# Kernel optimization log

Hardware: AMD Instinct MI355X
Metric: run time of the kernel (lower is better)

The kernel has to match this reference:

```python
import jax, jax.numpy as jnp
import numpy as np

N = 8192
D = 64
NUM_CLASSES = 100


def setup_inputs() -> dict:
    key = jax.random.key(0)
    k1, k2 = jax.random.split(key)
    output = jax.random.normal(k1, (N, D), dtype=jnp.float32)
    target = jax.random.randint(k2, (N,), 0, NUM_CLASSES, dtype=jnp.int64)
    return {"output": output, "target": target}


def reference(output, target):
    n = output.shape[0]
    # Pairwise similarity logits: [n, n]
    sim = output @ output.T
    # Upper-triangular (i < j) pair indices, static for jit.
    iu, ju = np.triu_indices(n, k=1)
    iu = jnp.asarray(iu)
    ju = jnp.asarray(ju)
    logits = sim[iu, ju]                                  # [n*(n-1)/2]
    labels = (target[iu] == target[ju]).astype(logits.dtype)
    # BCEWithLogits, mean reduction (numerically stable via log_sigmoid).
    loss = -(labels * jax.nn.log_sigmoid(logits)
             + (1.0 - labels) * jax.nn.log_sigmoid(-logits))
    return jnp.mean(loss)
```

## Files before the change

kernel.cpp:

```cpp
#include <hip/hip_runtime.h>

typedef __attribute__((ext_vector_type(8))) short bf16x8;
typedef __attribute__((ext_vector_type(4))) float floatx4;

namespace {
constexpr int kN = 8192;
constexpr int kD = 64;
constexpr int kTile = 128;
constexpr int kTilesPerDim = kN / kTile;
constexpr int kNumBlocks = kTilesPerDim * (kTilesPerDim + 1) / 2;
constexpr double kNumPairs = (double)kN * (double)(kN - 1) / 2.0;
__device__ __constant__ float kA1 = 0.99949556f;
__device__ __constant__ float kA2 = -0.49190896f;
__device__ __constant__ float kA3 = 0.28947478f;
__device__ __constant__ float kA4 = -0.13606275f;
__device__ __constant__ float kA5 = 0.03215845f;
constexpr float kNegLog2e = -1.4426950408889634f;
}

__device__ __forceinline__ short f2bf(float f) {
  unsigned u = __builtin_bit_cast(unsigned, f);
  unsigned r = u + 0x7FFFu + ((u >> 16) & 1u);
  return (short)(r >> 16);
}

__device__ __forceinline__ bf16x8 cvt8(const float4 f0, const float4 f1) {
  bf16x8 v;
  v[0] = f2bf(f0.x); v[1] = f2bf(f0.y); v[2] = f2bf(f0.z); v[3] = f2bf(f0.w);
  v[4] = f2bf(f1.x); v[5] = f2bf(f1.y); v[6] = f2bf(f1.z); v[7] = f2bf(f1.w);
  return v;
}

__device__ __forceinline__ float fast_exp2(float t) {
#if __has_builtin(__builtin_amdgcn_exp2f)
  return __builtin_amdgcn_exp2f(t);
#else
  return exp2f(t);
#endif
}

__global__ __launch_bounds__(256, 4) void pair_loss_kernel(
    const float* __restrict__ feat, const int* __restrict__ tgt,
    float* __restrict__ partial) {
  __shared__ short Bs[kTile * kD];
  __shared__ int Tcol[kTile];
  __shared__ float Red[4];

  const int bid = blockIdx.x;
  int by;
  {
    float f = 0.5f * (129.0f - sqrtf(16641.0f - 8.0f * (float)bid));
    by = (int)f;
    by = by > 63 ? 63 : (by < 0 ? 0 : by);
    while (64 * (by + 1) - ((by + 1) * by) / 2 <= bid) ++by;
    while (64 * by - (by * (by - 1)) / 2 > bid) --by;
  }
  const int bx = by + (bid - (64 * by - (by * (by - 1)) / 2));

  const int tid = threadIdx.x;
  const int lane = tid & 63;
  const int w = tid >> 6;
  const int quad = lane >> 4;
  const int l15 = lane & 15;
  const int l7 = lane & 7;

  {
    const int c = tid & 7;
    const int r0 = tid >> 3;
#pragma unroll
    for (int i = 0; i < 4; ++i) {
      const int r = r0 + 32 * i;
      const float* src = feat + (size_t)(bx * kTile + r) * kD + c * 8;
      const float4 f0 = *(const float4*)src;
      const float4 f1 = *(const float4*)(src + 4);
      *(bf16x8*)&Bs[r * kD + ((c ^ (r & 7)) << 3)] = cvt8(f0, f1);
    }
    if (tid < kTile) Tcol[tid] = tgt[bx * kTile + tid];
  }

  const int arow = by * kTile + w * 32;
  bf16x8 afrag[2][2];
#pragma unroll
  for (int rb = 0; rb < 2; ++rb) {
    const int row = arow + rb * 16 + l15;
#pragma unroll
    for (int ks = 0; ks < 2; ++ks) {
      const float* src = feat + (size_t)row * kD + ks * 32 + quad * 8;
      afrag[rb][ks] = cvt8(*(const float4*)src, *(const float4*)(src + 4));
    }
  }

  int trow[2][4];
#pragma unroll
  for (int rb = 0; rb < 2; ++rb) {
    const int4 t4 = *(const int4*)(tgt + arow + rb * 16 + quad * 4);
    trow[rb][0] = t4.x; trow[rb][1] = t4.y; trow[rb][2] = t4.z; trow[rb][3] = t4.w;
  }

  __syncthreads();

  float S_x = 0.0f, S_a = 0.0f, S_l = 0.0f, S_y = 0.0f;

#pragma unroll 2
  for (int cb = 0; cb < 8; ++cb) {
    const int R = cb * 16 + l15;
    const bf16x8 b0 = *(const bf16x8*)&Bs[R * kD + ((quad ^ l7) << 3)];
    const bf16x8 b1 = *(const bf16x8*)&Bs[R * kD + (((4 + quad) ^ l7) << 3)];
    floatx4 acc0 = {0.f, 0.f, 0.f, 0.f};
    floatx4 acc1 = {0.f, 0.f, 0.f, 0.f};
    acc0 = __builtin_amdgcn_mfma_f32_16x16x32_bf16(afrag[0][0], b0, acc0, 0, 0, 0);
    acc0 = __builtin_amdgcn_mfma_f32_16x16x32_bf16(afrag[0][1], b1, acc0, 0, 0, 0);
    acc1 = __builtin_amdgcn_mfma_f32_16x16x32_bf16(afrag[1][0], b0, acc1, 0, 0, 0);
    acc1 = __builtin_amdgcn_mfma_f32_16x16x32_bf16(afrag[1][1], b1, acc1, 0, 0, 0);

    const int tc = Tcol[R];
#pragma unroll
    for (int rb = 0; rb < 2; ++rb) {
      const floatx4 a = rb ? acc1 : acc0;
#pragma unroll
      for (int reg = 0; reg < 4; ++reg) {
        const float x = a[reg];
        S_x += x;
        S_a += fabsf(x);
        const float e = fast_exp2(kNegLog2e * fabsf(x));
        float h = fmaf(e, kA5, kA4);
        h = fmaf(e, h, kA3);
        h = fmaf(e, h, kA2);
        h = fmaf(e, h, kA1);
        S_l = fmaf(e, h, S_l);
        if (trow[rb][reg] == tc) S_y += x;
      }
    }
  }

  float lsum = 0.5f * (S_x + S_a) + S_l - S_y;

#pragma unroll
  for (int off = 32; off > 0; off >>= 1) lsum += __shfl_down(lsum, off);
  if (lane == 0) Red[w] = lsum;
  __syncthreads();
  if (tid == 0) {
    const float scale =
        (float)(1.0 / kNumPairs) * ((bx == by) ? 0.5f : 1.0f);
    partial[bid] = (Red[0] + Red[1] + Red[2] + Red[3]) * scale;
  }
}

__global__ void reduce_kernel(const float* __restrict__ partial,
                              float* __restrict__ out) {
  __shared__ float ws[4];
  const int tid = threadIdx.x;
  float s = 0.0f;
  for (int i = tid; i < kNumBlocks; i += 256) s += partial[i];
#pragma unroll
  for (int off = 32; off > 0; off >>= 1) s += __shfl_down(s, off);
  if ((tid & 63) == 0) ws[tid >> 6] = s;
  __syncthreads();
  if (tid == 0) out[0] = ws[0] + ws[1] + ws[2] + ws[3];
}

extern "C" void kernel_launch(void* const* d_in, const int* in_sizes, int n_in,
                              void* d_out, int out_size, void* d_ws,
                              size_t ws_size, hipStream_t stream) {
  const float* feat = (const float*)d_in[0];
  const int* tgt = (const int*)d_in[1];
  float* partial = (float*)d_ws;

  pair_loss_kernel<<<kNumBlocks, 256, 0, stream>>>(feat, tgt, partial);
  reduce_kernel<<<1, 256, 0, stream>>>(partial, (float*)d_out);
}
```

Measured before the change: 78.56 us.

## Replace per-pair label and linear terms with closed-form class-sum algebra

The linear parts of the loss (sum of x and the same-label sum of x) are computed algebraically from the feature sum vector and per-class feature sums, built by new class-sum and reduce kernels. This removes the per-pair target comparison and the per-element linear accumulation. The pair kernel now processes 128x256 tiles using a new block mapping that zero-weights tiles below the diagonal, and the final kernel combines the pieces. This adds two extra launches and shared-memory atomics, and introduces cancellation risk in float32 from subtracting large quadratic terms.

```diff
diff --git a/kernel.cpp b/kernel.cpp
--- a/kernel.cpp
+++ b/kernel.cpp
@@ -7,8 +7,9 @@
 constexpr int kN = 8192;
 constexpr int kD = 64;
 constexpr int kTile = 128;
-constexpr int kTilesPerDim = kN / kTile;
-constexpr int kNumBlocks = kTilesPerDim * (kTilesPerDim + 1) / 2;
+constexpr int kNumClasses = 100;
+constexpr int kNumBlocks = 1056;
+constexpr int kClsBlocks = 64;
 constexpr double kNumPairs = (double)kN * (double)(kN - 1) / 2.0;
 __device__ __constant__ float kA1 = 0.99949556f;
 __device__ __constant__ float kA2 = -0.49190896f;
@@ -16,6 +17,11 @@
 __device__ __constant__ float kA4 = -0.13606275f;
 __device__ __constant__ float kA5 = 0.03215845f;
 constexpr float kNegLog2e = -1.4426950408889634f;
+constexpr float kNegHalfLn2 = -0.34657359027997264f;
+constexpr int kOffG = 0;
+constexpr int kOffCls = 4096;
+constexpr int kOffSvec = kOffCls + kClsBlocks * kNumClasses * kD;
+constexpr int kOffClsSq = kOffSvec + kD;
 }
 
 __device__ __forceinline__ short f2bf(float f) {
@@ -39,23 +45,64 @@
 #endif
 }
 
+__global__ __launch_bounds__(256) void class_sum_kernel(
+    const float* __restrict__ feat, const int* __restrict__ tgt, float* ws) {
+  __shared__ float cls[kNumClasses * kD];
+  const int tid = threadIdx.x;
+  const int b = blockIdx.x;
+  for (int i = tid; i < kNumClasses * kD; i += 256) cls[i] = 0.0f;
+  if (b == 0 && tid < kD + 1) {
+    if (tid < kD) ws[kOffSvec + tid] = 0.0f;
+    else ws[kOffClsSq] = 0.0f;
+  }
+  __syncthreads();
+
+  const int row = b * 128 + (tid >> 1);
+  const int half = (tid & 1) * 32;
+  const int t = tgt[row];
+  const float* src = feat + (size_t)row * kD + half;
+#pragma unroll
+  for (int v = 0; v < 8; ++v) {
+    const float4 f = *(const float4*)(src + v * 4);
+    atomicAdd(&cls[t * kD + half + v * 4 + 0], f.x);
+    atomicAdd(&cls[t * kD + half + v * 4 + 1], f.y);
+    atomicAdd(&cls[t * kD + half + v * 4 + 2], f.z);
+    atomicAdd(&cls[t * kD + half + v * 4 + 3], f.w);
+  }
+  __syncthreads();
+  float* out = ws + kOffCls + (size_t)b * kNumClasses * kD;
+  for (int i = tid; i < kNumClasses * kD; i += 256) out[i] = cls[i];
+}
+
+__global__ __launch_bounds__(256) void class_reduce_kernel(float* ws) {
+  __shared__ float red[4];
+  const int tid = threadIdx.x;
+  const int gid = blockIdx.x * 256 + tid;
+  float s = 0.0f;
+  for (int b = 0; b < kClsBlocks; ++b)
+    s += ws[kOffCls + (size_t)b * kNumClasses * kD + gid];
+  atomicAdd(&ws[kOffSvec + (gid & (kD - 1))], s);
+  float q = s * s;
+#pragma unroll
+  for (int off = 32; off > 0; off >>= 1) q += __shfl_down(q, off);
+  if ((tid & 63) == 0) red[tid >> 6] = q;
+  __syncthreads();
+  if (tid == 0) atomicAdd(&ws[kOffClsSq], red[0] + red[1] + red[2] + red[3]);
+}
+
 __global__ __launch_bounds__(256, 4) void pair_loss_kernel(
-    const float* __restrict__ feat, const int* __restrict__ tgt,
-    float* __restrict__ partial) {
-  __shared__ short Bs[kTile * kD];
-  __shared__ int Tcol[kTile];
+    const float* __restrict__ feat, float* __restrict__ ws) {
+  __shared__ short Bs[256 * kD];
   __shared__ float Red[4];
 
   const int bid = blockIdx.x;
-  int by;
-  {
-    float f = 0.5f * (129.0f - sqrtf(16641.0f - 8.0f * (float)bid));
-    by = (int)f;
-    by = by > 63 ? 63 : (by < 0 ? 0 : by);
-    while (64 * (by + 1) - ((by + 1) * by) / 2 <= bid) ++by;
-    while (64 * by - (by * (by - 1)) / 2 > bid) --by;
-  }
-  const int bx = by + (bid - (64 * by - (by * (by - 1)) / 2));
+  int by = 0, start = 0;
+  while (start + (32 - (by >> 1)) <= bid) {
+    start += 32 - (by >> 1);
+    ++by;
+  }
+  const int sc = (by >> 1) + (bid - start);
+  const int bx0 = 2 * sc;
 
   const int tid = threadIdx.x;
   const int lane = tid & 63;
@@ -64,18 +111,15 @@
   const int l15 = lane & 15;
   const int l7 = lane & 7;
 
-  {
-    const int c = tid & 7;
-    const int r0 = tid >> 3;
-#pragma unroll
-    for (int i = 0; i < 4; ++i) {
-      const int r = r0 + 32 * i;
-      const float* src = feat + (size_t)(bx * kTile + r) * kD + c * 8;
-      const float4 f0 = *(const float4*)src;
-      const float4 f1 = *(const float4*)(src + 4);
-      *(bf16x8*)&Bs[r * kD + ((c ^ (r & 7)) << 3)] = cvt8(f0, f1);
-    }
-    if (tid < kTile) Tcol[tid] = tgt[bx * kTile + tid];
+#pragma unroll
+  for (int i = 0; i < 8; ++i) {
+    const int id = tid + 256 * i;
+    const int r = id >> 3;
+    const int c = id & 7;
+    const float* src = feat + (size_t)(bx0 * kTile + r) * kD + c * 8;
+    const float4 f0 = *(const float4*)src;
+    const float4 f1 = *(const float4*)(src + 4);
+    *(bf16x8*)&Bs[r * kD + ((c ^ (r & 7)) << 3)] = cvt8(f0, f1);
   }
 
   const int arow = by * kTile + w * 32;
@@ -90,22 +134,16 @@
     }
   }
 
-  int trow[2][4];
-#pragma unroll
-  for (int rb = 0; rb < 2; ++rb) {
-    const int4 t4 = *(const int4*)(tgt + arow + rb * 16 + quad * 4);
-    trow[rb][0] = t4.x; trow[rb][1] = t4.y; trow[rb][2] = t4.z; trow[rb][3] = t4.w;
-  }
-
-  __syncthreads();
-
-  float S_x = 0.0f, S_a = 0.0f, S_l = 0.0f, S_y = 0.0f;
+  __syncthreads();
+
+  float S_t0 = 0.0f, S_l0 = 0.0f, S_t1 = 0.0f, S_l1 = 0.0f;
 
 #pragma unroll 2
-  for (int cb = 0; cb < 8; ++cb) {
+  for (int cb = 0; cb < 16; ++cb) {
     const int R = cb * 16 + l15;
-    const bf16x8 b0 = *(const bf16x8*)&Bs[R * kD + ((quad ^ l7) << 3)];
-    const bf16x8 b1 = *(const bf16x8*)&Bs[R * kD + (((4 + quad) ^ l7) << 3)];
+    const int sw = R & 7;
+    const bf16x8 b0 = *(const bf16x8*)&Bs[R * kD + ((quad ^ sw) << 3)];
+    const bf16x8 b1 = *(const bf16x8*)&Bs[R * kD + (((4 + quad) ^ sw) << 3)];
     floatx4 acc0 = {0.f, 0.f, 0.f, 0.f};
     floatx4 acc1 = {0.f, 0.f, 0.f, 0.f};
     acc0 = __builtin_amdgcn_mfma_f32_16x16x32_bf16(afrag[0][0], b0, acc0, 0, 0, 0);
@@ -113,50 +151,63 @@
     acc1 = __builtin_amdgcn_mfma_f32_16x16x32_bf16(afrag[1][0], b0, acc1, 0, 0, 0);
     acc1 = __builtin_amdgcn_mfma_f32_16x16x32_bf16(afrag[1][1], b1, acc1, 0, 0, 0);
 
-    const int tc = Tcol[R];
+    float S_t = 0.0f, S_l = 0.0f;
 #pragma unroll
     for (int rb = 0; rb < 2; ++rb) {
       const floatx4 a = rb ? acc1 : acc0;
 #pragma unroll
       for (int reg = 0; reg < 4; ++reg) {
         const float x = a[reg];
-        S_x += x;
-        S_a += fabsf(x);
-        const float e = fast_exp2(kNegLog2e * fabsf(x));
+        const float t = kNegLog2e * fabsf(x);
+        S_t += t;
+        const float e = fast_exp2(t);
         float h = fmaf(e, kA5, kA4);
         h = fmaf(e, h, kA3);
         h = fmaf(e, h, kA2);
         h = fmaf(e, h, kA1);
         S_l = fmaf(e, h, S_l);
-        if (trow[rb][reg] == tc) S_y += x;
       }
     }
-  }
-
-  float lsum = 0.5f * (S_x + S_a) + S_l - S_y;
+    if (cb < 8) { S_t0 += S_t; S_l0 += S_l; }
+    else        { S_t1 += S_t; S_l1 += S_l; }
+  }
+
+  const float F0 = fmaf(kNegHalfLn2, S_t0, S_l0);
+  const float F1 = fmaf(kNegHalfLn2, S_t1, S_l1);
+  const float sc0 = (bx0 < by) ? 0.0f : ((bx0 == by) ? 0.5f : 1.0f);
+  const float sc1 = (bx0 + 1 == by) ? 0.5f : 1.0f;
+  float lsum = sc0 * F0 + sc1 * F1;
 
 #pragma unroll
   for (int off = 32; off > 0; off >>= 1) lsum += __shfl_down(lsum, off);
   if (lane == 0) Red[w] = lsum;
   __syncthreads();
+  if (tid == 0) ws[kOffG + bid] = Red[0] + Red[1] + Red[2] + Red[3];
+}
+
+__global__ __launch_bounds__(256) void final_kernel(const float* __restrict__ ws,
+                                                    float* __restrict__ out) {
+  __shared__ float red[4];
+  const int tid = threadIdx.x;
+  float s = 0.0f;
+  for (int i = tid; i < kNumBlocks; i += 256) s += ws[kOffG + i];
+  float q = (tid < kD) ? ws[kOffSvec + tid] : 0.0f;
+  q *= q;
+  float both[2] = {s, q};
+#pragma unroll
+  for (int k = 0; k < 2; ++k) {
+    float v = both[k];
+#pragma unroll
+    for (int off = 32; off > 0; off >>= 1) v += __shfl_down(v, off);
+    if ((tid & 63) == 0) red[tid >> 6] = v;
+    __syncthreads();
+    if (tid == 0) both[k] = red[0] + red[1] + red[2] + red[3];
+    __syncthreads();
+  }
   if (tid == 0) {
-    const float scale =
-        (float)(1.0 / kNumPairs) * ((bx == by) ? 0.5f : 1.0f);
-    partial[bid] = (Red[0] + Red[1] + Red[2] + Red[3]) * scale;
-  }
-}
-
-__global__ void reduce_kernel(const float* __restrict__ partial,
-                              float* __restrict__ out) {
-  __shared__ float ws[4];
-  const int tid = threadIdx.x;
-  float s = 0.0f;
-  for (int i = tid; i < kNumBlocks; i += 256) s += partial[i];
-#pragma unroll
-  for (int off = 32; off > 0; off >>= 1) s += __shfl_down(s, off);
-  if ((tid & 63) == 0) ws[tid >> 6] = s;
-  __syncthreads();
-  if (tid == 0) out[0] = ws[0] + ws[1] + ws[2] + ws[3];
+    const float G = both[0], SS = both[1];
+    out[0] = (G + 0.25f * SS - 0.5f * ws[kOffClsSq]) * (float)(1.0 / kNumPairs);
+  }
 }
 
 extern "C" void kernel_launch(void* const* d_in, const int* in_sizes, int n_in,
@@ -164,8 +215,10 @@
                               size_t ws_size, hipStream_t stream) {
   const float* feat = (const float*)d_in[0];
   const int* tgt = (const int*)d_in[1];
-  float* partial = (float*)d_ws;
-
-  pair_loss_kernel<<<kNumBlocks, 256, 0, stream>>>(feat, tgt, partial);
-  reduce_kernel<<<1, 256, 0, stream>>>(partial, (float*)d_out);
-}
+  float* ws = (float*)d_ws;
+
+  class_sum_kernel<<<kClsBlocks, 256, 0, stream>>>(feat, tgt, ws);
+  pair_loss_kernel<<<kNumBlocks, 256, 0, stream>>>(feat, ws);
+  class_reduce_kernel<<<kNumClasses * kD / 256, 256, 0, stream>>>(ws);
+  final_kernel<<<1, 256, 0, stream>>>(ws, (float*)d_out);
+}
```

Result: slower. 94.25 us (+20.0%).
